# Performance work log

Hardware: AMD Instinct MI355X
Metric: run time of the kernel (lower is better)

The kernel has to match this reference:

```python
import jax, jax.numpy as jnp
import numpy as np

B, S, C = 16, 2048, 1024
H = 8            # preference_dim / num_heads
HD = C // H      # head_dim = 128


def setup_inputs() -> dict:
    key = jax.random.key(0)
    ks = jax.random.split(key, 8)
    s1 = 1.0 / np.sqrt(1.0)   # Linear(1, HD) init scale (not critical)
    sh = 1.0 / np.sqrt(HD)
    return {
        "features": jax.random.normal(ks[0], (B, S, C), dtype=jnp.float32),
        "preference": jax.random.normal(ks[1], (B, H), dtype=jnp.float32),
        "Wq": jax.random.uniform(ks[2], (HD, 1), jnp.float32, -s1, s1),
        "bq": jax.random.uniform(ks[3], (HD,), jnp.float32, -s1, s1),
        "Wk": jax.random.uniform(ks[4], (HD, HD), jnp.float32, -sh, sh),
        "bk": jax.random.uniform(ks[5], (HD,), jnp.float32, -sh, sh),
        "Wv": jax.random.uniform(ks[6], (HD, HD), jnp.float32, -sh, sh),
        "bv": jax.random.uniform(ks[7], (HD,), jnp.float32, -sh, sh),
    }


def reference(features, preference, Wq, bq, Wk, bk, Wv, bv):
    b, s, c = features.shape
    h, hd = H, HD
    # query: Linear(1->hd) applied to per-head scalar preference; constant over step
    # q[b,h,d] = preference[b,h] * Wq[d,0] + bq[d]
    q = preference[:, :, None] * Wq[:, 0][None, None, :] + bq  # [B,H,HD]
    f = features.reshape(b, s, h, hd)                          # head slices
    k = jnp.einsum('bshd,ed->bshe', f, Wk) + bk                # [B,S,H,HD]
    v = jnp.einsum('bshd,ed->bshe', f, Wv) + bv                # [B,S,H,HD]
    # original builds [B,S,S] scores per head, but query rows are identical
    # across step, so softmax(q @ k^T) @ v has identical rows; compute once.
    scores = jnp.einsum('bhd,bshd->bhs', q, k)                 # [B,H,S]
    attn = jax.nn.softmax(scores, axis=-1)
    ctx = jnp.einsum('bhs,bshd->bhd', attn, v)                 # [B,H,HD]
    weighted = jnp.broadcast_to(ctx[:, None, :, :], (b, s, h, hd)).reshape(b, s, c)
    return weighted + features
```

## Files before the change

kernel.cpp:

```cpp
#include <hip/hip_runtime.h>
#include <math.h>

#define B 16
#define S 2048
#define C 1024
#define H 8
#define HD 128

__global__ void k1_qk(const float* __restrict__ pref, const float* __restrict__ Wq,
                      const float* __restrict__ bq, const float* __restrict__ Wk,
                      float* __restrict__ qk) {
    int bh = blockIdx.x;
    int d  = threadIdx.x;
    __shared__ float qsh[HD];
    float p = pref[bh];
    qsh[d] = p * Wq[d] + bq[d];
    __syncthreads();
    float s = 0.f;
#pragma unroll 8
    for (int e = 0; e < HD; ++e)
        s += qsh[e] * Wk[e * HD + d];
    qk[bh * HD + d] = s;
}

__global__ __launch_bounds__(256) void k2_pass(
    const float* __restrict__ feat, const float* __restrict__ qk,
    float* __restrict__ pm, float* __restrict__ pl, float* __restrict__ pf,
    int NC, int R) {
    int wg    = blockIdx.x;
    int b     = wg / NC;
    int chunk = wg - b * NC;
    int t     = threadIdx.x;
    int h     = t >> 5;
    int lane32 = t & 31;

    const float4* frow = (const float4*)feat
                       + (size_t)(b * S + chunk * R) * (C / 4) + t;
    float4 qv = ((const float4*)qk)[(b * H + h) * (HD / 4) + lane32];

    float m = -1e30f, l = 0.f;
    float a0 = 0.f, a1 = 0.f, a2 = 0.f, a3 = 0.f;

    for (int s = 0; s < R; ++s) {
        float4 f = frow[(size_t)s * (C / 4)];
        float part = f.x * qv.x + f.y * qv.y + f.z * qv.z + f.w * qv.w;
        part += __shfl_xor(part, 16, 32);
        part += __shfl_xor(part, 8, 32);
        part += __shfl_xor(part, 4, 32);
        part += __shfl_xor(part, 2, 32);
        part += __shfl_xor(part, 1, 32);
        float mn    = fmaxf(m, part);
        float scale = __expf(m - mn);
        float p     = __expf(part - mn);
        l  = l * scale + p;
        a0 = a0 * scale + p * f.x;
        a1 = a1 * scale + p * f.y;
        a2 = a2 * scale + p * f.z;
        a3 = a3 * scale + p * f.w;
        m  = mn;
    }
    if (lane32 == 0) { pm[wg * H + h] = m; pl[wg * H + h] = l; }
    float4 o; o.x = a0; o.y = a1; o.z = a2; o.w = a3;
    ((float4*)pf)[(size_t)wg * (C / 4) + t] = o;
}

__global__ __launch_bounds__(128) void k3_combine(
    const float* __restrict__ pm, const float* __restrict__ pl,
    const float* __restrict__ pf, const float* __restrict__ Wv,
    const float* __restrict__ bv, float* __restrict__ ctx, int NC) {
    int bh = blockIdx.x;
    int b = bh >> 3, h = bh & 7;
    int t = threadIdx.x;
    __shared__ float wsh[64];
    __shared__ float fsh[HD];

    float M = -1e30f;
    for (int i = 0; i < NC; ++i)
        M = fmaxf(M, pm[(b * NC + i) * H + h]);
    if (t < NC) wsh[t] = __expf(pm[(b * NC + t) * H + h] - M);
    __syncthreads();
    float L = 0.f;
    for (int i = 0; i < NC; ++i)
        L += pl[(b * NC + i) * H + h] * wsh[i];
    float acc = 0.f;
    for (int i = 0; i < NC; ++i)
        acc += pf[(size_t)(b * NC + i) * C + h * HD + t] * wsh[i];
    fsh[t] = acc / L;
    __syncthreads();
    float s = 0.f;
#pragma unroll 8
    for (int d = 0; d < HD; ++d)
        s += fsh[d] * Wv[t * HD + d];
    ctx[bh * HD + t] = s + bv[t];
}

__global__ __launch_bounds__(256) void k4_epilogue(
    const float* __restrict__ feat, const float* __restrict__ ctx,
    float* __restrict__ out) {
    size_t i = (size_t)blockIdx.x * blockDim.x + threadIdx.x;
    float4 f = ((const float4*)feat)[i];
    size_t b  = i >> 19;
    size_t c4 = i & 255;
    float4 cv = ((const float4*)ctx)[b * (C / 4) + c4];
    float4 o; o.x = f.x + cv.x; o.y = f.y + cv.y;
    o.z = f.z + cv.z; o.w = f.w + cv.w;
    ((float4*)out)[i] = o;
}

extern "C" void kernel_launch(void* const* d_in, const int* in_sizes, int n_in,
                              void* d_out, int out_size, void* d_ws, size_t ws_size,
                              hipStream_t stream) {
    const float* feat = (const float*)d_in[0];
    const float* pref = (const float*)d_in[1];
    const float* Wq   = (const float*)d_in[2];
    const float* bq   = (const float*)d_in[3];
    const float* Wk   = (const float*)d_in[4];
    const float* Wv   = (const float*)d_in[6];
    const float* bv   = (const float*)d_in[7];
    float* out = (float*)d_out;

    int NC = 64;
    auto need = [](int nc) {
        return (size_t)(B * H * HD + B * C + 2 * B * nc * H + (size_t)B * nc * C) * 4;
    };
    while (NC > 1 && need(NC) > ws_size) NC >>= 1;
    int R = S / NC;

    float* ws  = (float*)d_ws;
    float* qk  = ws;
    float* ctx = qk + B * H * HD;
    float* pm  = ctx + B * C;
    float* pl  = pm + B * NC * H;
    float* pf  = pl + B * NC * H;

    k1_qk<<<B * H, HD, 0, stream>>>(pref, Wq, bq, Wk, qk);
    k2_pass<<<B * NC, 256, 0, stream>>>(feat, qk, pm, pl, pf, NC, R);
    k3_combine<<<B * H, HD, 0, stream>>>(pm, pl, pf, Wv, bv, ctx, NC);
    k4_epilogue<<<(B * S * C / 4) / 256, 256, 0, stream>>>(feat, ctx, out);
}
```

Before: 292.7 us.

## Fuse query-key projection into streaming pass, batch row loads, grid-stride epilogue

```diff
diff --git a/kernel.cpp b/kernel.cpp
--- a/kernel.cpp
+++ b/kernel.cpp
@@ -6,83 +6,93 @@
 #define C 1024
 #define H 8
 #define HD 128
-
-__global__ void k1_qk(const float* __restrict__ pref, const float* __restrict__ Wq,
-                      const float* __restrict__ bq, const float* __restrict__ Wk,
-                      float* __restrict__ qk) {
-    int bh = blockIdx.x;
-    int d  = threadIdx.x;
-    __shared__ float qsh[HD];
-    float p = pref[bh];
-    qsh[d] = p * Wq[d] + bq[d];
-    __syncthreads();
-    float s = 0.f;
-#pragma unroll 8
-    for (int e = 0; e < HD; ++e)
-        s += qsh[e] * Wk[e * HD + d];
-    qk[bh * HD + d] = s;
-}
+#define NC 64
+#define R (S / NC)
 
 __global__ __launch_bounds__(256) void k2_pass(
-    const float* __restrict__ feat, const float* __restrict__ qk,
-    float* __restrict__ pm, float* __restrict__ pl, float* __restrict__ pf,
-    int NC, int R) {
+    const float* __restrict__ feat, const float* __restrict__ pref,
+    const float* __restrict__ Wq, const float* __restrict__ bq,
+    const float* __restrict__ Wk,
+    float* __restrict__ pm, float* __restrict__ pl, float* __restrict__ pf) {
     int wg    = blockIdx.x;
-    int b     = wg / NC;
-    int chunk = wg - b * NC;
+    int b     = wg >> 6;
+    int chunk = wg & (NC - 1);
     int t     = threadIdx.x;
     int h     = t >> 5;
     int lane32 = t & 31;
 
+    float p = pref[b * H + h];
+    float4 qv; qv.x = qv.y = qv.z = qv.w = 0.f;
+    const float4* Wk4 = (const float4*)Wk;
+#pragma unroll 8
+    for (int e = 0; e < HD; ++e) {
+        float qe = p * Wq[e] + bq[e];
+        float4 w = Wk4[e * (HD / 4) + lane32];
+        qv.x += qe * w.x; qv.y += qe * w.y;
+        qv.z += qe * w.z; qv.w += qe * w.w;
+    }
+
     const float4* frow = (const float4*)feat
                        + (size_t)(b * S + chunk * R) * (C / 4) + t;
-    float4 qv = ((const float4*)qk)[(b * H + h) * (HD / 4) + lane32];
+    float m = -1e30f, l = 0.f;
+    float4 a; a.x = a.y = a.z = a.w = 0.f;
 
-    float m = -1e30f, l = 0.f;
-    float a0 = 0.f, a1 = 0.f, a2 = 0.f, a3 = 0.f;
-
-    for (int s = 0; s < R; ++s) {
-        float4 f = frow[(size_t)s * (C / 4)];
-        float part = f.x * qv.x + f.y * qv.y + f.z * qv.z + f.w * qv.w;
-        part += __shfl_xor(part, 16, 32);
-        part += __shfl_xor(part, 8, 32);
-        part += __shfl_xor(part, 4, 32);
-        part += __shfl_xor(part, 2, 32);
-        part += __shfl_xor(part, 1, 32);
-        float mn    = fmaxf(m, part);
-        float scale = __expf(m - mn);
-        float p     = __expf(part - mn);
-        l  = l * scale + p;
-        a0 = a0 * scale + p * f.x;
-        a1 = a1 * scale + p * f.y;
-        a2 = a2 * scale + p * f.z;
-        a3 = a3 * scale + p * f.w;
-        m  = mn;
+#pragma unroll
+    for (int s0 = 0; s0 < R; s0 += 4) {
+        float4 f[4]; float sc[4];
+#pragma unroll
+        for (int j = 0; j < 4; ++j)
+            f[j] = frow[(size_t)(s0 + j) * (C / 4)];
+#pragma unroll
+        for (int j = 0; j < 4; ++j) {
+            float part = f[j].x * qv.x + f[j].y * qv.y
+                       + f[j].z * qv.z + f[j].w * qv.w;
+            part += __shfl_xor(part, 16, 32);
+            part += __shfl_xor(part, 8, 32);
+            part += __shfl_xor(part, 4, 32);
+            part += __shfl_xor(part, 2, 32);
+            part += __shfl_xor(part, 1, 32);
+            sc[j] = part;
+        }
+#pragma unroll
+        for (int j = 0; j < 4; ++j) {
+            float mn    = fmaxf(m, sc[j]);
+            float scale = __expf(m - mn);
+            float pw    = __expf(sc[j] - mn);
+            l   = l * scale + pw;
+            a.x = a.x * scale + pw * f[j].x;
+            a.y = a.y * scale + pw * f[j].y;
+            a.z = a.z * scale + pw * f[j].z;
+            a.w = a.w * scale + pw * f[j].w;
+            m   = mn;
+        }
     }
     if (lane32 == 0) { pm[wg * H + h] = m; pl[wg * H + h] = l; }
-    float4 o; o.x = a0; o.y = a1; o.z = a2; o.w = a3;
-    ((float4*)pf)[(size_t)wg * (C / 4) + t] = o;
+    ((float4*)pf)[(size_t)wg * (C / 4) + t] = a;
 }
 
 __global__ __launch_bounds__(128) void k3_combine(
     const float* __restrict__ pm, const float* __restrict__ pl,
     const float* __restrict__ pf, const float* __restrict__ Wv,
-    const float* __restrict__ bv, float* __restrict__ ctx, int NC) {
+    const float* __restrict__ bv, float* __restrict__ ctx) {
     int bh = blockIdx.x;
     int b = bh >> 3, h = bh & 7;
     int t = threadIdx.x;
-    __shared__ float wsh[64];
+    __shared__ float wsh[NC];
     __shared__ float fsh[HD];
 
     float M = -1e30f;
+#pragma unroll 8
     for (int i = 0; i < NC; ++i)
         M = fmaxf(M, pm[(b * NC + i) * H + h]);
     if (t < NC) wsh[t] = __expf(pm[(b * NC + t) * H + h] - M);
     __syncthreads();
     float L = 0.f;
+#pragma unroll 8
     for (int i = 0; i < NC; ++i)
         L += pl[(b * NC + i) * H + h] * wsh[i];
     float acc = 0.f;
+#pragma unroll 8
     for (int i = 0; i < NC; ++i)
         acc += pf[(size_t)(b * NC + i) * C + h * HD + t] * wsh[i];
     fsh[t] = acc / L;
@@ -97,14 +107,18 @@
 __global__ __launch_bounds__(256) void k4_epilogue(
     const float* __restrict__ feat, const float* __restrict__ ctx,
     float* __restrict__ out) {
-    size_t i = (size_t)blockIdx.x * blockDim.x + threadIdx.x;
-    float4 f = ((const float4*)feat)[i];
-    size_t b  = i >> 19;
-    size_t c4 = i & 255;
-    float4 cv = ((const float4*)ctx)[b * (C / 4) + c4];
-    float4 o; o.x = f.x + cv.x; o.y = f.y + cv.y;
-    o.z = f.z + cv.z; o.w = f.w + cv.w;
-    ((float4*)out)[i] = o;
+    constexpr int N4 = B * S * C / 4;
+    int tid = blockIdx.x * 256 + threadIdx.x;
+    int nth = gridDim.x * 256;
+    for (int i = tid; i < N4; i += nth) {
+        float4 f = ((const float4*)feat)[i];
+        int b  = i >> 19;
+        int c4 = i & 255;
+        float4 cv = ((const float4*)ctx)[b * (C / 4) + c4];
+        float4 o; o.x = f.x + cv.x; o.y = f.y + cv.y;
+        o.z = f.z + cv.z; o.w = f.w + cv.w;
+        ((float4*)out)[i] = o;
+    }
 }
 
 extern "C" void kernel_launch(void* const* d_in, const int* in_sizes, int n_in,
@@ -119,22 +133,13 @@
     const float* bv   = (const float*)d_in[7];
     float* out = (float*)d_out;
 
-    int NC = 64;
-    auto need = [](int nc) {
-        return (size_t)(B * H * HD + B * C + 2 * B * nc * H + (size_t)B * nc * C) * 4;
-    };
-    while (NC > 1 && need(NC) > ws_size) NC >>= 1;
-    int R = S / NC;
-
     float* ws  = (float*)d_ws;
-    float* qk  = ws;
-    float* ctx = qk + B * H * HD;
+    float* ctx = ws;
     float* pm  = ctx + B * C;
     float* pl  = pm + B * NC * H;
     float* pf  = pl + B * NC * H;
 
-    k1_qk<<<B * H, HD, 0, stream>>>(pref, Wq, bq, Wk, qk);
-    k2_pass<<<B * NC, 256, 0, stream>>>(feat, qk, pm, pl, pf, NC, R);
-    k3_combine<<<B * H, HD, 0, stream>>>(pm, pl, pf, Wv, bv, ctx, NC);
-    k4_epilogue<<<(B * S * C / 4) / 256, 256, 0, stream>>>(feat, ctx, out);
+    k2_pass<<<B * NC, 256, 0, stream>>>(feat, pref, Wq, bq, Wk, pm, pl, pf);
+    k3_combine<<<B * H, 128, 0, stream>>>(pm, pl, pf, Wv, bv, ctx);
+    k4_epilogue<<<4096, 256, 0, stream>>>(feat, ctx, out);
 }
```

Result: slower. 318.4 us (+8.8%).
